# Kernel tuning notes

Measured on AMD Instinct MI355X. Metric: run time of the kernel, lower is better.

Reference implementation:

```python
import jax, jax.numpy as jnp
import numpy as np

N, K = 16384, 1024  # samples, classes == feature dim


def setup_inputs() -> dict:
    key = jax.random.key(0)
    k1, k2 = jax.random.split(key)
    x = jax.random.normal(k1, (N, K), dtype=jnp.float32)
    # mu initialized like 100*one_hot plus noise so normalization is non-trivial
    mu = 100.0 * jnp.eye(K, dtype=jnp.float32) + jax.random.normal(k2, (K, K), dtype=jnp.float32)
    std = jnp.full((K,), 1.0 / K, dtype=jnp.float32)  # diag(eye(K)) * 1/K
    return {"x": x, "mu": mu, "std": std}


def reference(x, mu, std):
    # mu normalized per-row (as in forward)
    mu_n = mu / jnp.linalg.norm(mu, axis=-1, keepdims=True)  # [M, K]
    inv_std = 1.0 / std  # [K]
    # Mahalanobis-style squared distance with diagonal covariance, via GEMM expansion:
    xx = (x * x) @ inv_std                                  # [N]
    mm = jnp.sum(mu_n * mu_n * inv_std[None, :], axis=-1)   # [M]
    cross = x @ (mu_n * inv_std[None, :]).T                 # [N, M]
    logits = -0.5 * (xx[:, None] + mm[None, :] - 2.0 * cross)
    return logits
```

## Files before the change

kernel.cpp:

```cpp
#include <hip/hip_runtime.h>

typedef __attribute__((ext_vector_type(8))) int   i32x8;
typedef __attribute__((ext_vector_type(4))) float f32x4;
typedef unsigned int uint32;

constexpr int N = 16384;
constexpr int K = 1024;
constexpr int M = 1024;

#define WAITVM(n) asm volatile("s_waitcnt vmcnt(" #n ")" ::: "memory")
#define FENCE() asm volatile("" ::: "memory")
#define BAR()                          \
    do {                               \
        FENCE();                       \
        __builtin_amdgcn_s_barrier();  \
        FENCE();                       \
    } while (0)

__device__ inline void gload_lds16(const unsigned char* g, unsigned char* l) {
    __builtin_amdgcn_global_load_lds(
        (const __attribute__((address_space(1))) unsigned int*)g,
        (__attribute__((address_space(3))) unsigned int*)l,
        16, 0, 0);
}

__device__ inline uint32 pack4_fp8(float a, float b, float c, float d) {
    int v = __builtin_amdgcn_cvt_pk_fp8_f32(a, b, 0, false);
    v = __builtin_amdgcn_cvt_pk_fp8_f32(c, d, v, true);
    return (uint32)v;
}

__global__ void prep_mu(const float* __restrict__ mu, const float* __restrict__ stdv,
                        unsigned char* __restrict__ Bp, float* __restrict__ mmh) {
    int m = blockIdx.x;
    int t = threadIdx.x;
    float4 v = ((const float4*)(mu + (size_t)m * K))[t];
    float4 s = ((const float4*)stdv)[t];
    float ix = 1.0f / s.x, iy = 1.0f / s.y, iz = 1.0f / s.z, iw = 1.0f / s.w;
    float sum2  = v.x * v.x + v.y * v.y + v.z * v.z + v.w * v.w;
    float sum2w = v.x * v.x * ix + v.y * v.y * iy + v.z * v.z * iz + v.w * v.w * iw;
    for (int off = 32; off > 0; off >>= 1) {
        sum2  += __shfl_down(sum2, off, 64);
        sum2w += __shfl_down(sum2w, off, 64);
    }
    __shared__ float r2[4], r2w[4];
    __shared__ float s_scale;
    int lane = t & 63, w = t >> 6;
    if (lane == 0) { r2[w] = sum2; r2w[w] = sum2w; }
    __syncthreads();
    if (t == 0) {
        float tot2  = r2[0] + r2[1] + r2[2] + r2[3];
        float tot2w = r2w[0] + r2w[1] + r2w[2] + r2w[3];
        mmh[m] = -0.5f * tot2w / tot2;
        s_scale = rsqrtf(tot2) * 0.25f;
    }
    __syncthreads();
    float sc = s_scale;
    int col0 = t * 4;
    int kt = col0 >> 7;
    int lk = (col0 >> 5) & 3;
    int j  = col0 & 31;
    int fl = (m & 15) + lk * 16;
    int g  = m >> 4;
    uint32* dst = (uint32*)(Bp + ((size_t)((g * 8 + kt) * 64 + fl)) * 32 + j);
    *dst = pack4_fp8(v.x * ix * sc, v.y * iy * sc, v.z * iz * sc, v.w * iw * sc);
}

__global__ __launch_bounds__(256) void prep_x(const float* __restrict__ x,
                                              const float* __restrict__ stdv,
                                              uint32* __restrict__ xb8,
                                              float* __restrict__ xxh) {
    int row = blockIdx.x * 4 + (threadIdx.x >> 6);
    int lane = threadIdx.x & 63;
    const float4* src = (const float4*)(x + (size_t)row * K);
    const float4* sp  = (const float4*)stdv;
    uint32* dst = xb8 + (size_t)row * (K / 4);
    float ssum = 0.f;
#pragma unroll
    for (int i = 0; i < 4; ++i) {
        int idx = lane + 64 * i;
        float4 v = src[idx];
        float4 s = sp[idx];
        ssum += v.x * v.x / s.x + v.y * v.y / s.y + v.z * v.z / s.z + v.w * v.w / s.w;
        dst[idx] = pack4_fp8(v.x, v.y, v.z, v.w);
    }
#pragma unroll
    for (int off = 32; off > 0; off >>= 1) ssum += __shfl_down(ssum, off, 64);
    if (lane == 0) xxh[row] = -0.5f * ssum;
}

#define BKB 128
#define ATILE (128 * BKB)

__global__ __launch_bounds__(256, 3) void gemm_ep(
    const unsigned char* __restrict__ A8, const unsigned char* __restrict__ Bp,
    const float* __restrict__ xxh, const float* __restrict__ mmh,
    float* __restrict__ C) {
    __shared__ unsigned char Als[2 * ATILE];

    int t = threadIdx.x;
    int lane = t & 63;
    int wave = t >> 6;
    int wr = wave >> 1;
    int wc = wave & 1;
    int r  = lane & 15;
    int lk = lane >> 4;

    int bid = blockIdx.x;
    int swz = (bid & 7) * 128 + (bid >> 3);
    int tn = swz >> 3;
    int tm = swz & 7;

    const unsigned char* Abase = A8 + (size_t)tn * 128 * K;
    const unsigned char* Bw = Bp + (size_t)(tm * 8 + wc * 4) * 16384 + (size_t)lane * 32;

    f32x4 acc[4][4] = {};
    i32x8 af[4], bf[4];

#define STAGE_A(kt_, buf_)                                                     \
    {                                                                          \
        const unsigned char* g_ = Abase + (size_t)(kt_) * BKB;                 \
        unsigned char* l_ = Als + (buf_) * ATILE;                              \
        _Pragma("unroll")                                                      \
        for (int i_ = 0; i_ < 4; ++i_) {                                       \
            int c_ = i_ * 256 + t;                                             \
            int row_ = c_ >> 3;                                                \
            int slot_ = (c_ & 7) ^ (row_ & 7);                                 \
            gload_lds16(g_ + (size_t)row_ * K + slot_ * 16,                    \
                        l_ + (i_ * 256 + (wave << 6)) * 16);                   \
        }                                                                      \
    }

    STAGE_A(0, 0);
    WAITVM(0);
    BAR();

    const int NT = K / BKB;
    for (int kt = 0; kt < NT; ++kt) {
        int cur = kt & 1;
        const unsigned char* As = Als + cur * ATILE;

#pragma unroll
        for (int ni = 0; ni < 4; ++ni) {
            const unsigned char* gb = Bw + (size_t)ni * 16384 + (size_t)kt * 2048;
            uint4 q0 = *(const uint4*)gb;
            uint4 q1 = *(const uint4*)(gb + 16);
            bf[ni][0] = q0.x; bf[ni][1] = q0.y; bf[ni][2] = q0.z; bf[ni][3] = q0.w;
            bf[ni][4] = q1.x; bf[ni][5] = q1.y; bf[ni][6] = q1.z; bf[ni][7] = q1.w;
        }

        if (kt + 1 < NT) STAGE_A(kt + 1, cur ^ 1);

#pragma unroll
        for (int mi = 0; mi < 4; ++mi) {
            int row = wr * 64 + mi * 16 + r;
            uint4 q0 = *(const uint4*)&As[(row << 7) + ((((lk << 1) | 0) ^ (r & 7)) << 4)];
            uint4 q1 = *(const uint4*)&As[(row << 7) + ((((lk << 1) | 1) ^ (r & 7)) << 4)];
            af[mi][0] = q0.x; af[mi][1] = q0.y; af[mi][2] = q0.z; af[mi][3] = q0.w;
            af[mi][4] = q1.x; af[mi][5] = q1.y; af[mi][6] = q1.z; af[mi][7] = q1.w;
        }

        __builtin_amdgcn_s_setprio(1);
#pragma unroll
        for (int mi = 0; mi < 4; ++mi)
#pragma unroll
            for (int ni = 0; ni < 4; ++ni)
                acc[mi][ni] = __builtin_amdgcn_mfma_scale_f32_16x16x128_f8f6f4(
                    af[mi], bf[ni], acc[mi][ni],
                    0, 0,
                    0, 0x7f7f7f7f,
                    0, 0x7f7f7f7f);
        __builtin_amdgcn_s_setprio(0);

        if (kt + 1 < NT) WAITVM(0);
        BAR();
    }

    int rowb = tn * 128 + wr * 64;
    int colb = tm * 128 + wc * 64;
#pragma unroll
    for (int mi = 0; mi < 4; ++mi) {
        float xh[4];
#pragma unroll
        for (int j = 0; j < 4; ++j) xh[j] = xxh[rowb + mi * 16 + lk * 4 + j];
#pragma unroll
        for (int ni = 0; ni < 4; ++ni) {
            int col = colb + ni * 16 + r;
            float mh = mmh[col];
#pragma unroll
            for (int j = 0; j < 4; ++j) {
                int row = rowb + mi * 16 + lk * 4 + j;
                C[(size_t)row * M + col] = acc[mi][ni][j] * 4.0f + xh[j] + mh;
            }
        }
    }
#undef STAGE_A
}

extern "C" void kernel_launch(void* const* d_in, const int* in_sizes, int n_in,
                              void* d_out, int out_size, void* d_ws, size_t ws_size,
                              hipStream_t stream) {
    const float* x    = (const float*)d_in[0];
    const float* mu   = (const float*)d_in[1];
    const float* stdv = (const float*)d_in[2];
    float* out = (float*)d_out;

    char* ws = (char*)d_ws;
    unsigned char* xb8 = (unsigned char*)ws;
    unsigned char* Bp  = (unsigned char*)(ws + (size_t)N * K);
    float* xxh = (float*)(ws + (size_t)N * K + (size_t)M * K);
    float* mmh = (float*)((char*)xxh + (size_t)N * sizeof(float));

    prep_mu<<<M, 256, 0, stream>>>(mu, stdv, Bp, mmh);
    prep_x<<<N / 4, 256, 0, stream>>>(x, stdv, (uint32*)xb8, xxh);
    gemm_ep<<<(N / 128) * (M / 128), 256, 0, stream>>>(xb8, Bp, xxh, mmh, out);
}
```

Before: 52.55 us.

## Fuse x FP8 quantization and row-norm into GEMM, drop prep_x kernel

Result: slower. 58.31 us (+11.0%).

```diff
diff --git a/kernel.cpp b/kernel.cpp
--- a/kernel.cpp
+++ b/kernel.cpp
@@ -8,8 +8,12 @@
 constexpr int K = 1024;
 constexpr int M = 1024;
 
-#define WAITVM(n) asm volatile("s_waitcnt vmcnt(" #n ")" ::: "memory")
 #define FENCE() asm volatile("" ::: "memory")
+#define WAITLGKM0_PIN()                                    \
+    do {                                                   \
+        asm volatile("s_waitcnt lgkmcnt(0)" ::: "memory"); \
+        __builtin_amdgcn_sched_barrier(0);                 \
+    } while (0)
 #define BAR()                          \
     do {                               \
         FENCE();                       \
@@ -17,13 +21,6 @@
         FENCE();                       \
     } while (0)
 
-__device__ inline void gload_lds16(const unsigned char* g, unsigned char* l) {
-    __builtin_amdgcn_global_load_lds(
-        (const __attribute__((address_space(1))) unsigned int*)g,
-        (__attribute__((address_space(3))) unsigned int*)l,
-        16, 0, 0);
-}
-
 __device__ inline uint32 pack4_fp8(float a, float b, float c, float d) {
     int v = __builtin_amdgcn_cvt_pk_fp8_f32(a, b, 0, false);
     v = __builtin_amdgcn_cvt_pk_fp8_f32(c, d, v, true);
@@ -31,12 +28,17 @@
 }
 
 __global__ void prep_mu(const float* __restrict__ mu, const float* __restrict__ stdv,
-                        unsigned char* __restrict__ Bp, float* __restrict__ mmh) {
+                        unsigned char* __restrict__ Bp, float* __restrict__ mmh,
+                        float* __restrict__ istd) {
     int m = blockIdx.x;
     int t = threadIdx.x;
     float4 v = ((const float4*)(mu + (size_t)m * K))[t];
     float4 s = ((const float4*)stdv)[t];
     float ix = 1.0f / s.x, iy = 1.0f / s.y, iz = 1.0f / s.z, iw = 1.0f / s.w;
+    if (m == 0) {
+        float4* o = (float4*)(istd + t * 4);
+        *o = make_float4(ix, iy, iz, iw);
+    }
     float sum2  = v.x * v.x + v.y * v.y + v.z * v.z + v.w * v.w;
     float sum2w = v.x * v.x * ix + v.y * v.y * iy + v.z * v.z * iz + v.w * v.w * iw;
     for (int off = 32; off > 0; off >>= 1) {
@@ -66,35 +68,11 @@
     *dst = pack4_fp8(v.x * ix * sc, v.y * iy * sc, v.z * iz * sc, v.w * iw * sc);
 }
 
-__global__ __launch_bounds__(256) void prep_x(const float* __restrict__ x,
-                                              const float* __restrict__ stdv,
-                                              uint32* __restrict__ xb8,
-                                              float* __restrict__ xxh) {
-    int row = blockIdx.x * 4 + (threadIdx.x >> 6);
-    int lane = threadIdx.x & 63;
-    const float4* src = (const float4*)(x + (size_t)row * K);
-    const float4* sp  = (const float4*)stdv;
-    uint32* dst = xb8 + (size_t)row * (K / 4);
-    float ssum = 0.f;
-#pragma unroll
-    for (int i = 0; i < 4; ++i) {
-        int idx = lane + 64 * i;
-        float4 v = src[idx];
-        float4 s = sp[idx];
-        ssum += v.x * v.x / s.x + v.y * v.y / s.y + v.z * v.z / s.z + v.w * v.w / s.w;
-        dst[idx] = pack4_fp8(v.x, v.y, v.z, v.w);
-    }
-#pragma unroll
-    for (int off = 32; off > 0; off >>= 1) ssum += __shfl_down(ssum, off, 64);
-    if (lane == 0) xxh[row] = -0.5f * ssum;
-}
-
-#define BKB 128
-#define ATILE (128 * BKB)
-
-__global__ __launch_bounds__(256, 3) void gemm_ep(
-    const unsigned char* __restrict__ A8, const unsigned char* __restrict__ Bp,
-    const float* __restrict__ xxh, const float* __restrict__ mmh,
+#define ATILE 16384
+
+__global__ __launch_bounds__(256, 2) void gemm_ep(
+    const float* __restrict__ x, const unsigned char* __restrict__ Bp,
+    const float* __restrict__ istd, const float* __restrict__ mmh,
     float* __restrict__ C) {
     __shared__ unsigned char Als[2 * ATILE];
 
@@ -111,90 +89,165 @@
     int tn = swz >> 3;
     int tm = swz & 7;
 
-    const unsigned char* Abase = A8 + (size_t)tn * 128 * K;
+    const float* Xp = x + (size_t)tn * 128 * K;
     const unsigned char* Bw = Bp + (size_t)(tm * 8 + wc * 4) * 16384 + (size_t)lane * 32;
 
+    int colblk = t & 15;
+    int rowblk = t >> 4;
+    const float* xthr = Xp + (size_t)rowblk * 8 * K + colblk * 8;
+
     f32x4 acc[4][4] = {};
+    float xxp[8] = {0.f, 0.f, 0.f, 0.f, 0.f, 0.f, 0.f, 0.f};
+    uint32 pk[16];
+    float4 xa0, xa1, xa2, xa3, xa4, xa5, xa6, xa7, sda, sdb;
     i32x8 af[4], bf[4];
 
-#define STAGE_A(kt_, buf_)                                                     \
-    {                                                                          \
-        const unsigned char* g_ = Abase + (size_t)(kt_) * BKB;                 \
+#define ISSUE_H(kt2_, h_)                                                      \
+    {                                                                          \
+        const float* gx_ = xthr + (size_t)(h_) * 4 * K + (size_t)(kt2_) * 128; \
+        xa0 = *(const float4*)(gx_ + 0 * K);                                   \
+        xa1 = *(const float4*)(gx_ + 0 * K + 4);                               \
+        xa2 = *(const float4*)(gx_ + 1 * K);                                   \
+        xa3 = *(const float4*)(gx_ + 1 * K + 4);                               \
+        xa4 = *(const float4*)(gx_ + 2 * K);                                   \
+        xa5 = *(const float4*)(gx_ + 2 * K + 4);                               \
+        xa6 = *(const float4*)(gx_ + 3 * K);                                   \
+        xa7 = *(const float4*)(gx_ + 3 * K + 4);                               \
+        if ((h_) == 0) {                                                       \
+            sda = *(const float4*)(istd + (kt2_) * 128 + colblk * 8);          \
+            sdb = *(const float4*)(istd + (kt2_) * 128 + colblk * 8 + 4);      \
+        }                                                                      \
+    }
+
+#define PROC_ROW(ri_, va_, vb_)                                                \
+    xxp[ri_] += va_.x * va_.x * sda.x + va_.y * va_.y * sda.y +                \
+                va_.z * va_.z * sda.z + va_.w * va_.w * sda.w +                \
+                vb_.x * vb_.x * sdb.x + vb_.y * vb_.y * sdb.y +                \
+                vb_.z * vb_.z * sdb.z + vb_.w * vb_.w * sdb.w;                 \
+    pk[(ri_) * 2]     = pack4_fp8(va_.x, va_.y, va_.z, va_.w);                 \
+    pk[(ri_) * 2 + 1] = pack4_fp8(vb_.x, vb_.y, vb_.z, vb_.w);
+
+#define PROCESS_H(h_)                                                          \
+    {                                                                          \
+        PROC_ROW((h_) * 4 + 0, xa0, xa1);                                      \
+        PROC_ROW((h_) * 4 + 1, xa2, xa3);                                      \
+        PROC_ROW((h_) * 4 + 2, xa4, xa5);                                      \
+        PROC_ROW((h_) * 4 + 3, xa6, xa7);                                      \
+    }
+
+#define DSW(buf_)                                                              \
+    {                                                                          \
         unsigned char* l_ = Als + (buf_) * ATILE;                              \
         _Pragma("unroll")                                                      \
-        for (int i_ = 0; i_ < 4; ++i_) {                                       \
-            int c_ = i_ * 256 + t;                                             \
-            int row_ = c_ >> 3;                                                \
-            int slot_ = (c_ & 7) ^ (row_ & 7);                                 \
-            gload_lds16(g_ + (size_t)row_ * K + slot_ * 16,                    \
-                        l_ + (i_ * 256 + (wave << 6)) * 16);                   \
+        for (int ri_ = 0; ri_ < 8; ++ri_) {                                    \
+            int gr_ = rowblk * 8 + ri_;                                        \
+            int ba_ = gr_ * 128 + ((((colblk >> 1)) ^ (gr_ & 7)) << 4) +       \
+                      ((colblk & 1) << 3);                                     \
+            *(uint2*)(l_ + ba_) = make_uint2(pk[ri_ * 2], pk[ri_ * 2 + 1]);    \
         }                                                                      \
     }
 
-    STAGE_A(0, 0);
-    WAITVM(0);
+#define BFL(kt_)                                                               \
+    _Pragma("unroll")                                                          \
+    for (int ni_ = 0; ni_ < 4; ++ni_) {                                        \
+        const unsigned char* gb_ =                                             \
+            Bw + (size_t)ni_ * 16384 + (size_t)(kt_) * 2048;                   \
+        uint4 q0_ = *(const uint4*)gb_;                                        \
+        uint4 q1_ = *(const uint4*)(gb_ + 16);                                 \
+        bf[ni_][0] = q0_.x; bf[ni_][1] = q0_.y;                                \
+        bf[ni_][2] = q0_.z; bf[ni_][3] = q0_.w;                                \
+        bf[ni_][4] = q1_.x; bf[ni_][5] = q1_.y;                                \
+        bf[ni_][6] = q1_.z; bf[ni_][7] = q1_.w;                                \
+    }
+
+#define AFL(buf_)                                                              \
+    {                                                                          \
+        const unsigned char* As_ = Als + (buf_) * ATILE;                       \
+        _Pragma("unroll")                                                      \
+        for (int mi_ = 0; mi_ < 4; ++mi_) {                                    \
+            int row_ = wr * 64 + mi_ * 16 + r;                                 \
+            uint4 q0_ = *(const uint4*)&As_[(row_ << 7) +                      \
+                        ((((lk << 1) | 0) ^ (r & 7)) << 4)];                   \
+            uint4 q1_ = *(const uint4*)&As_[(row_ << 7) +                      \
+                        ((((lk << 1) | 1) ^ (r & 7)) << 4)];                   \
+            af[mi_][0] = q0_.x; af[mi_][1] = q0_.y;                            \
+            af[mi_][2] = q0_.z; af[mi_][3] = q0_.w;                            \
+            af[mi_][4] = q1_.x; af[mi_][5] = q1_.y;                            \
+            af[mi_][6] = q1_.z; af[mi_][7] = q1_.w;                            \
+        }                                                                      \
+    }
+
+#define MFMA_H(h_)                                                             \
+    __builtin_amdgcn_s_setprio(1);                                             \
+    _Pragma("unroll")                                                          \
+    for (int mi_ = (h_) * 2; mi_ < (h_) * 2 + 2; ++mi_)                        \
+        _Pragma("unroll")                                                      \
+        for (int ni_ = 0; ni_ < 4; ++ni_)                                      \
+            acc[mi_][ni_] = __builtin_amdgcn_mfma_scale_f32_16x16x128_f8f6f4(  \
+                af[mi_], bf[ni_], acc[mi_][ni_],                               \
+                0, 0, 0, 0x7f7f7f7f, 0, 0x7f7f7f7f);                           \
+    __builtin_amdgcn_s_setprio(0);
+
+    ISSUE_H(0, 0); PROCESS_H(0);
+    ISSUE_H(0, 1); PROCESS_H(1);
+    DSW(0);
+    ISSUE_H(1, 0); PROCESS_H(0);
+    ISSUE_H(1, 1); PROCESS_H(1);
+    WAITLGKM0_PIN();
     BAR();
 
-    const int NT = K / BKB;
-    for (int kt = 0; kt < NT; ++kt) {
+    for (int kt = 0; kt < 8; ++kt) {
         int cur = kt & 1;
-        const unsigned char* As = Als + cur * ATILE;
-
-#pragma unroll
-        for (int ni = 0; ni < 4; ++ni) {
-            const unsigned char* gb = Bw + (size_t)ni * 16384 + (size_t)kt * 2048;
-            uint4 q0 = *(const uint4*)gb;
-            uint4 q1 = *(const uint4*)(gb + 16);
-            bf[ni][0] = q0.x; bf[ni][1] = q0.y; bf[ni][2] = q0.z; bf[ni][3] = q0.w;
-            bf[ni][4] = q1.x; bf[ni][5] = q1.y; bf[ni][6] = q1.z; bf[ni][7] = q1.w;
-        }
-
-        if (kt + 1 < NT) STAGE_A(kt + 1, cur ^ 1);
-
-#pragma unroll
-        for (int mi = 0; mi < 4; ++mi) {
-            int row = wr * 64 + mi * 16 + r;
-            uint4 q0 = *(const uint4*)&As[(row << 7) + ((((lk << 1) | 0) ^ (r & 7)) << 4)];
-            uint4 q1 = *(const uint4*)&As[(row << 7) + ((((lk << 1) | 1) ^ (r & 7)) << 4)];
-            af[mi][0] = q0.x; af[mi][1] = q0.y; af[mi][2] = q0.z; af[mi][3] = q0.w;
-            af[mi][4] = q1.x; af[mi][5] = q1.y; af[mi][6] = q1.z; af[mi][7] = q1.w;
-        }
-
-        __builtin_amdgcn_s_setprio(1);
-#pragma unroll
-        for (int mi = 0; mi < 4; ++mi)
-#pragma unroll
-            for (int ni = 0; ni < 4; ++ni)
-                acc[mi][ni] = __builtin_amdgcn_mfma_scale_f32_16x16x128_f8f6f4(
-                    af[mi], bf[ni], acc[mi][ni],
-                    0, 0,
-                    0, 0x7f7f7f7f,
-                    0, 0x7f7f7f7f);
-        __builtin_amdgcn_s_setprio(0);
-
-        if (kt + 1 < NT) WAITVM(0);
+        if (kt < 7) DSW(cur ^ 1);
+        BFL(kt);
+        if (kt < 6) ISSUE_H(kt + 2, 0);
+        AFL(cur);
+        MFMA_H(0);
+        if (kt < 6) { PROCESS_H(0); ISSUE_H(kt + 2, 1); }
+        MFMA_H(1);
+        if (kt < 6) PROCESS_H(1);
+        WAITLGKM0_PIN();
         BAR();
     }
+
+    float* xsc = (float*)Als;
+#pragma unroll
+    for (int ri = 0; ri < 8; ++ri)
+        xsc[(rowblk * 8 + ri) * 17 + colblk] = xxp[ri];
+    WAITLGKM0_PIN();
+    BAR();
+    float* xrow = (float*)(Als + 128 * 17 * 4);
+    if (t < 128) {
+        float s_ = 0.f;
+#pragma unroll
+        for (int c = 0; c < 16; ++c) s_ += xsc[t * 17 + c];
+        xrow[t] = -0.5f * s_;
+    }
+    WAITLGKM0_PIN();
+    BAR();
 
     int rowb = tn * 128 + wr * 64;
     int colb = tm * 128 + wc * 64;
 #pragma unroll
     for (int mi = 0; mi < 4; ++mi) {
-        float xh[4];
-#pragma unroll
-        for (int j = 0; j < 4; ++j) xh[j] = xxh[rowb + mi * 16 + lk * 4 + j];
+        float4 xh = *(const float4*)&xrow[wr * 64 + mi * 16 + lk * 4];
 #pragma unroll
         for (int ni = 0; ni < 4; ++ni) {
             int col = colb + ni * 16 + r;
             float mh = mmh[col];
-#pragma unroll
-            for (int j = 0; j < 4; ++j) {
-                int row = rowb + mi * 16 + lk * 4 + j;
-                C[(size_t)row * M + col] = acc[mi][ni][j] * 4.0f + xh[j] + mh;
-            }
+            C[(size_t)(rowb + mi * 16 + lk * 4 + 0) * M + col] = acc[mi][ni][0] * 4.0f + xh.x + mh;
+            C[(size_t)(rowb + mi * 16 + lk * 4 + 1) * M + col] = acc[mi][ni][1] * 4.0f + xh.y + mh;
+            C[(size_t)(rowb + mi * 16 + lk * 4 + 2) * M + col] = acc[mi][ni][2] * 4.0f + xh.z + mh;
+            C[(size_t)(rowb + mi * 16 + lk * 4 + 3) * M + col] = acc[mi][ni][3] * 4.0f + xh.w + mh;
         }
     }
-#undef STAGE_A
+#undef ISSUE_H
+#undef PROC_ROW
+#undef PROCESS_H
+#undef DSW
+#undef BFL
+#undef AFL
+#undef MFMA_H
 }
 
 extern "C" void kernel_launch(void* const* d_in, const int* in_sizes, int n_in,
@@ -206,12 +259,10 @@
     float* out = (float*)d_out;
 
     char* ws = (char*)d_ws;
-    unsigned char* xb8 = (unsigned char*)ws;
-    unsigned char* Bp  = (unsigned char*)(ws + (size_t)N * K);
-    float* xxh = (float*)(ws + (size_t)N * K + (size_t)M * K);
-    float* mmh = (float*)((char*)xxh + (size_t)N * sizeof(float));
-
-    prep_mu<<<M, 256, 0, stream>>>(mu, stdv, Bp, mmh);
-    prep_x<<<N / 4, 256, 0, stream>>>(x, stdv, (uint32*)xb8, xxh);
-    gemm_ep<<<(N / 128) * (M / 128), 256, 0, stream>>>(xb8, Bp, xxh, mmh, out);
-}
+    unsigned char* Bp  = (unsigned char*)ws;
+    float* mmh  = (float*)(ws + (size_t)M * K);
+    float* istd = (float*)(ws + (size_t)M * K + 4096);
+
+    prep_mu<<<M, 256, 0, stream>>>(mu, stdv, Bp, mmh, istd);
+    gemm_ep<<<(N / 128) * (M / 128), 256, 0, stream>>>(x, Bp, istd, mmh, out);
+}
```
